# Kernel optimization log

Hardware: AMD Instinct MI355X
Metric: run time of the kernel (lower is better)

Reference implementation:

```python
import jax, jax.numpy as jnp
import numpy as np

EPS = 1e-6
NUM_GROUPS = 16


def group_norm(x, gamma, beta):
    # x: [B, C, H, W]
    B, C, H, W = x.shape
    xg = x.reshape(B, NUM_GROUPS, C // NUM_GROUPS, H, W)
    mean = xg.mean(axis=(2, 3, 4), keepdims=True)
    var = xg.var(axis=(2, 3, 4), keepdims=True)
    xg = (xg - mean) * jax.lax.rsqrt(var + EPS)
    x = xg.reshape(B, C, H, W)
    return x * gamma[None, :, None, None] + beta[None, :, None, None]


def conv1x1(x, w, b):
    # x: [B, C, H, W], w: [O, C], b: [O]
    return jnp.einsum('bchw,oc->bohw', x, w) + b[None, :, None, None]


def setup_inputs() -> dict:
    key = jax.random.key(0)
    ks = jax.random.split(key, 6)
    B, C, H, W = 8, 256, 64, 64
    s = 1.0 / np.sqrt(C)
    return {
        'x': jax.random.normal(ks[0], (B, C, H, W), dtype=jnp.float32),
        'gamma': jnp.ones((C,), jnp.float32),
        'beta': jnp.zeros((C,), jnp.float32),
        'wq': jax.random.normal(ks[1], (C, C), dtype=jnp.float32) * s,
        'bq': jnp.zeros((C,), jnp.float32),
        'wk': jax.random.normal(ks[2], (C, C), dtype=jnp.float32) * s,
        'bk': jnp.zeros((C,), jnp.float32),
        'wv': jax.random.normal(ks[3], (C, C), dtype=jnp.float32) * s,
        'bv': jnp.zeros((C,), jnp.float32),
        'wp': jax.random.normal(ks[4], (C, C), dtype=jnp.float32) * s,
        'bp': jnp.zeros((C,), jnp.float32),
    }


def reference(x, gamma, beta, wq, bq, wk, bk, wv, bv, wp, bp):
    B, C, H, W = x.shape
    identity = x
    h = group_norm(x, gamma, beta)
    q = conv1x1(h, wq, bq).reshape(B, C, H * W)  # [B, C, N]
    k = conv1x1(h, wk, bk).reshape(B, C, H * W)
    v = conv1x1(h, wv, bv).reshape(B, C, H * W)
    # alpha[b, i, j] = sum_c q[b, c, i] * k[b, c, j], scaled by C^-0.5
    alpha = jnp.einsum('bci,bcj->bij', q, k) * (C ** -0.5)
    alpha = jax.nn.softmax(alpha, axis=-1)
    # out[b, c, i] = sum_j v[b, c, j] * alpha[b, i, j]
    out = jnp.einsum('bcj,bij->bci', v, alpha).reshape(B, C, H, W)
    out = conv1x1(out, wp, bp)
    return identity + out
```

## Files before the change

kernel.cpp:

```cpp
#include <hip/hip_runtime.h>
#include <hip/hip_bf16.h>


typedef unsigned int u32;
typedef unsigned short u16;
typedef __bf16 bf16x8 __attribute__((ext_vector_type(8)));
typedef float f32x4 __attribute__((ext_vector_type(4)));
typedef float f32x16 __attribute__((ext_vector_type(16)));

#define GAS __attribute__((address_space(1)))
#define LAS __attribute__((address_space(3)))

__device__ __forceinline__ u16 f2bf(float f) {
  union { float f; u32 u; } v; v.f = f;
  return (u16)((v.u + 0x7fffu + ((v.u >> 16) & 1u)) >> 16);
}

__device__ __forceinline__ f32x16 mfma32(bf16x8 a, bf16x8 b, f32x16 c) {
  return __builtin_amdgcn_mfma_f32_32x32x16_bf16(a, b, c, 0, 0, 0);
}

template<int ITERS, int NT>
__device__ __forceinline__ void stage_lin(u16* lds, const u16* g, int tid) {
#pragma unroll
  for (int it = 0; it < ITERS; ++it) {
    int idx = it * NT + tid;
    const u16* src = g + (long)idx * 8;
    u16* dst = lds + (long)(idx & ~63) * 8;
    __builtin_amdgcn_global_load_lds((const GAS u32*)src, (LAS u32*)dst, 16, 0, 0);
  }
}

template<int ROWS, int NT>
__device__ __forceinline__ void stage_gran(u16* lds, const u16* g, int k0, int tid) {
  constexpr int ITERS = 4 * ROWS / NT;
#pragma unroll
  for (int it = 0; it < ITERS; ++it) {
    int gi = it * NT + tid;
    int row = gi & (ROWS - 1);
    int kh = gi / ROWS;
    const u16* src = g + (long)row * 256 + k0 + kh * 8;
    u16* dst = lds + (long)(gi & ~63) * 8;
    __builtin_amdgcn_global_load_lds((const GAS u32*)src, (LAS u32*)dst, 16, 0, 0);
  }
}

__global__ __launch_bounds__(256) void convert_w(
    const float* __restrict__ w0, const float* __restrict__ w1,
    const float* __restrict__ w2, const float* __restrict__ w3,
    u16* __restrict__ out) {
  int i = blockIdx.x * 256 + threadIdx.x;
  int seg = i >> 16, idx = i & 65535;
  const float* w = seg == 0 ? w0 : seg == 1 ? w1 : seg == 2 ? w2 : w3;
  out[i] = f2bf(w[idx]);
}

__global__ __launch_bounds__(256) void gn_kernel(
    const float* __restrict__ x, const float* __restrict__ gamma,
    const float* __restrict__ beta, u16* __restrict__ ht) {
  int tid = threadIdx.x;
  int b = blockIdx.x >> 4;
  int grp = blockIdx.x & 15;
  const float* xg = x + ((long)b * 256 + grp * 16) * 4096;

  float s = 0.f, ss = 0.f;
  const float4* x4 = (const float4*)xg;
#pragma unroll 4
  for (int it = 0; it < 64; ++it) {
    float4 v = x4[it * 256 + tid];
    s += v.x + v.y + v.z + v.w;
    ss += v.x * v.x + v.y * v.y + v.z * v.z + v.w * v.w;
  }
#pragma unroll
  for (int d = 1; d < 64; d <<= 1) {
    s += __shfl_xor(s, d);
    ss += __shfl_xor(ss, d);
  }
  __shared__ float red[10];
  int lane = tid & 63, wave = tid >> 6;
  if (lane == 0) { red[wave] = s; red[4 + wave] = ss; }
  __syncthreads();
  if (tid == 0) {
    float S = red[0] + red[1] + red[2] + red[3];
    float SS = red[4] + red[5] + red[6] + red[7];
    float mean = S * (1.f / 65536.f);
    float var = SS * (1.f / 65536.f) - mean * mean;
    red[8] = mean;
    red[9] = rsqrtf(var + 1e-6f);
  }
  __syncthreads();
  float mean = red[8], rstd = red[9];

  float a[16], bb[16];
#pragma unroll
  for (int c = 0; c < 16; ++c) {
    float gm = gamma[grp * 16 + c];
    float bt = beta[grp * 16 + c];
    a[c] = gm * rstd;
    bb[c] = bt - mean * a[c];
  }
  u16* hb = ht + (long)b * 4096 * 256 + grp * 16;
  for (int it = 0; it < 16; ++it) {
    int n = it * 256 + tid;
    __align__(16) u16 tmp[16];
#pragma unroll
    for (int c = 0; c < 16; ++c)
      tmp[c] = f2bf(xg[(long)c * 4096 + n] * a[c] + bb[c]);
    u16* dst = hb + (long)n * 256;
    ((uint4*)dst)[0] = ((uint4*)tmp)[0];
    ((uint4*)dst)[1] = ((uint4*)tmp)[1];
  }
}

__global__ __launch_bounds__(256, 2) void gemm_qkv(
    const u16* __restrict__ ht, const u16* __restrict__ wbf,
    u16* __restrict__ qtb, u16* __restrict__ ktb, u16* __restrict__ vcb,
    const float* __restrict__ bq, const float* __restrict__ bk,
    const float* __restrict__ bv) {
  __shared__ __align__(16) u16 as2[4 * 128 * 8];
  __shared__ __align__(16) u16 bs2[3][4 * 128 * 8];

  int tid = threadIdx.x;
  int lane = tid & 63;
  int h = lane >> 5, lr = lane & 31;
  int wave = tid >> 6;
  int wp = wave >> 1, wo = wave & 1;
  long mrow = (long)blockIdx.x * 128;
  int ob = blockIdx.y * 128;

  f32x16 zero16 = {0,0,0,0,0,0,0,0,0,0,0,0,0,0,0,0};
  f32x16 acc[3][2][2];
#pragma unroll
  for (int m = 0; m < 3; ++m)
#pragma unroll
    for (int p = 0; p < 2; ++p)
#pragma unroll
      for (int q = 0; q < 2; ++q) acc[m][p][q] = zero16;

  const u16* Ab = ht + mrow * 256;

  for (int step = 0; step < 8; ++step) {
    int k0 = step * 32;
    __syncthreads();
    stage_gran<128, 256>(as2, Ab, k0, tid);
    stage_gran<128, 256>(bs2[0], wbf + (long)ob * 256, k0, tid);
    stage_gran<128, 256>(bs2[1], wbf + 65536 + (long)ob * 256, k0, tid);
    stage_gran<128, 256>(bs2[2], wbf + 131072 + (long)ob * 256, k0, tid);
    __syncthreads();

#pragma unroll
    for (int ks = 0; ks < 2; ++ks) {
      int kg = (2 * ks + h) * 128;
      bf16x8 a0 = *(const bf16x8*)(as2 + (long)(kg + wp * 64 + lr) * 8);
      bf16x8 a1 = *(const bf16x8*)(as2 + (long)(kg + wp * 64 + 32 + lr) * 8);
      __builtin_amdgcn_s_setprio(1);
#pragma unroll
      for (int m = 0; m < 3; ++m) {
        bf16x8 b0 = *(const bf16x8*)(bs2[m] + (long)(kg + wo * 64 + lr) * 8);
        bf16x8 b1 = *(const bf16x8*)(bs2[m] + (long)(kg + wo * 64 + 32 + lr) * 8);
        acc[m][0][0] = mfma32(a0, b0, acc[m][0][0]);
        acc[m][0][1] = mfma32(a0, b1, acc[m][0][1]);
        acc[m][1][0] = mfma32(a1, b0, acc[m][1][0]);
        acc[m][1][1] = mfma32(a1, b1, acc[m][1][1]);
      }
      __builtin_amdgcn_s_setprio(0);
    }
  }

  const float QSC = 0.0625f * 1.44269504f;
  long b_ = mrow >> 12;
  int posb = (int)(mrow & 4095);
#pragma unroll
  for (int p = 0; p < 2; ++p)
#pragma unroll
    for (int q = 0; q < 2; ++q) {
      int o = ob + wo * 64 + q * 32 + lr;
      float bqv = bq[o], bkv = bk[o], bvv = bv[o];
      int posl0 = posb + wp * 64 + p * 32;
      int jt = posl0 >> 5;
      long tbase = b_ * 1048576 + (long)jt * 8192;
      long kbase = tbase + (o >> 3) * 256 + (o & 7);
      long vbase = tbase + (long)o * 8;
      long qrow0 = (mrow + wp * 64 + p * 32) * 256 + o;
#pragma unroll
      for (int quad = 0; quad < 4; ++quad) {
        __align__(8) u16 v4[4];
#pragma unroll
        for (int e = 0; e < 4; ++e) {
          int rloc = 8 * quad + 4 * h + e;
          float vq = acc[0][p][q][4 * quad + e];
          float vk = acc[1][p][q][4 * quad + e];
          float vv = acc[2][p][q][4 * quad + e];
          qtb[qrow0 + (long)rloc * 256] = f2bf((vq + bqv) * QSC);
          ktb[kbase + rloc * 8] = f2bf(vk + bkv);
          v4[e] = f2bf(vv + bvv);
        }
        int r0 = 8 * quad + 4 * h;
        *(uint2*)(vcb + vbase + ((r0 >> 3) & 3) * 2048 + (r0 & 7)) = *(uint2*)v4;
      }
    }
}

__global__ __launch_bounds__(256) void gemm_proj(
    const u16* __restrict__ Wp, const u16* __restrict__ ao,
    float* __restrict__ outp, const float* __restrict__ bias,
    const float* __restrict__ resid) {
  __shared__ __align__(16) u16 ws2[4 * 256 * 8];
  __shared__ __align__(16) u16 aos[4 * 64 * 8];

  int tid = threadIdx.x;
  int lane = tid & 63;
  int h = lane >> 5, lr = lane & 31;
  int wo = tid >> 6;
  long b = blockIdx.x & 7;
  int pos0 = (blockIdx.x >> 3) * 64;
  const u16* aob = ao + (b * 4096 + pos0) * 256;

  f32x16 zero16 = {0,0,0,0,0,0,0,0,0,0,0,0,0,0,0,0};
  f32x16 acc[2][2];
#pragma unroll
  for (int p = 0; p < 2; ++p)
#pragma unroll
    for (int q = 0; q < 2; ++q) acc[p][q] = zero16;

  for (int step = 0; step < 8; ++step) {
    int k0 = step * 32;
    __syncthreads();
    stage_gran<256, 256>(ws2, Wp, k0, tid);
    stage_gran<64, 256>(aos, aob, k0, tid);
    __syncthreads();

#pragma unroll
    for (int ks = 0; ks < 2; ++ks) {
      int kgw = (2 * ks + h) * 256;
      int kga = (2 * ks + h) * 64;
      bf16x8 w0 = *(const bf16x8*)(ws2 + (long)(kgw + wo * 64 + lr) * 8);
      bf16x8 w1 = *(const bf16x8*)(ws2 + (long)(kgw + wo * 64 + 32 + lr) * 8);
      bf16x8 o0 = *(const bf16x8*)(aos + (long)(kga + lr) * 8);
      bf16x8 o1 = *(const bf16x8*)(aos + (long)(kga + 32 + lr) * 8);
      __builtin_amdgcn_s_setprio(1);
      acc[0][0] = mfma32(w0, o0, acc[0][0]);
      acc[0][1] = mfma32(w0, o1, acc[0][1]);
      acc[1][0] = mfma32(w1, o0, acc[1][0]);
      acc[1][1] = mfma32(w1, o1, acc[1][1]);
      __builtin_amdgcn_s_setprio(0);
    }
  }

#pragma unroll
  for (int p = 0; p < 2; ++p)
#pragma unroll
    for (int q = 0; q < 2; ++q) {
      int pos = pos0 + q * 32 + lr;
#pragma unroll
      for (int quad = 0; quad < 4; ++quad)
#pragma unroll
        for (int e = 0; e < 4; ++e) {
          int o = wo * 64 + p * 32 + 8 * quad + 4 * h + e;
          long addr = b * 1048576 + (long)o * 4096 + pos;
          outp[addr] = acc[p][q][4 * quad + e] + bias[o] + resid[addr];
        }
    }
}

__global__ __launch_bounds__(256, 2) void attn_flash(
    const u16* __restrict__ qt, const u16* __restrict__ kgp,
    const u16* __restrict__ vgp, u16* __restrict__ part0, u16* __restrict__ part1,
    float2* __restrict__ ml0, float2* __restrict__ ml1) {
  __shared__ __align__(16) u16 ksT[2 * 8192];
  __shared__ __align__(16) u16 vsT[2 * 8192];
  __shared__ float fws[128];

  int tid = threadIdx.x;
  int lane = tid & 63;
  int h = lane >> 5, lr = lane & 31;
  int rg = tid >> 6;
  int bid = blockIdx.x;
  long b = bid & 7;
  int jhalf = (bid >> 3) & 1;
  int i0 = (bid >> 4) * 128;

  const u16* kb = kgp + b * 1048576 + (long)(jhalf * 64) * 8192;
  const u16* vb = vgp + b * 1048576 + (long)(jhalf * 64) * 8192;
  float* fw = fws + rg * 32;

  const u16* qrow = qt + ((b * 4096 + i0 + rg * 32 + lr) << 8) + h * 8;
  bf16x8 qreg[16];
#pragma unroll
  for (int kk = 0; kk < 16; ++kk)
    qreg[kk] = *(const bf16x8*)(qrow + kk * 16);

  f32x16 zero16 = {0,0,0,0,0,0,0,0,0,0,0,0,0,0,0,0};
  f32x16 acc[8];
#pragma unroll
  for (int ct = 0; ct < 8; ++ct) acc[ct] = zero16;
  float mrun = -3e38f, lsum = 0.f;

  stage_lin<4, 256>(ksT, kb, tid);
  stage_lin<4, 256>(vsT, vb, tid);

  for (int t = 0; t < 64; ++t) {
    int cur = t & 1, nxt = cur ^ 1;
    __builtin_amdgcn_s_barrier();
    __builtin_amdgcn_sched_barrier(0);
    if (t < 63) {
      stage_lin<4, 256>(ksT + nxt * 8192, kb + (long)(t + 1) * 8192, tid);
      stage_lin<4, 256>(vsT + nxt * 8192, vb + (long)(t + 1) * 8192, tid);
    }
    __builtin_amdgcn_sched_barrier(0);
    asm volatile("s_waitcnt vmcnt(8)" ::: "memory");
    __builtin_amdgcn_sched_barrier(0);
    __builtin_amdgcn_s_barrier();
    __builtin_amdgcn_sched_barrier(0);

    const u16* ksl = ksT + cur * 8192;
    const u16* vsl = vsT + cur * 8192;

    f32x16 sacc = zero16;
    __builtin_amdgcn_s_setprio(1);
#pragma unroll
    for (int kk = 0; kk < 16; ++kk) {
      bf16x8 kf = *(const bf16x8*)(ksl + ((2 * kk + h) * 32 + lr) * 8);
      sacc = mfma32(kf, qreg[kk], sacc);
    }
    __builtin_amdgcn_s_setprio(0);

    float m0 = fmaxf(fmaxf(sacc[0], sacc[1]), fmaxf(sacc[2], sacc[3]));
    float m1 = fmaxf(fmaxf(sacc[4], sacc[5]), fmaxf(sacc[6], sacc[7]));
    float m2 = fmaxf(fmaxf(sacc[8], sacc[9]), fmaxf(sacc[10], sacc[11]));
    float m3 = fmaxf(fmaxf(sacc[12], sacc[13]), fmaxf(sacc[14], sacc[15]));
    float mloc = fmaxf(fmaxf(m0, m1), fmaxf(m2, m3));
    mloc = fmaxf(mloc, __shfl_xor(mloc, 32));

    if (!__all(mloc - mrun <= 8.f)) {
      float mnew = fmaxf(mrun, mloc);
      float al = exp2f(mrun - mnew);
      mrun = mnew;
      lsum *= al;
      if (h == 0) fw[lr] = al;
      asm volatile("s_waitcnt lgkmcnt(0)" ::: "memory");
      f32x4 fq0 = *(const f32x4*)&fw[4 * h];
      f32x4 fq1 = *(const f32x4*)&fw[8 + 4 * h];
      f32x4 fq2 = *(const f32x4*)&fw[16 + 4 * h];
      f32x4 fq3 = *(const f32x4*)&fw[24 + 4 * h];
      f32x16 alv;
#pragma unroll
      for (int e = 0; e < 4; ++e) {
        alv[e] = fq0[e]; alv[4 + e] = fq1[e]; alv[8 + e] = fq2[e]; alv[12 + e] = fq3[e];
      }
#pragma unroll
      for (int ct = 0; ct < 8; ++ct) acc[ct] *= alv;
    }

    u32 u[8];
#pragma unroll
    for (int m = 0; m < 8; ++m) {
      float p0 = exp2f(sacc[2 * m] - mrun);
      float p1 = exp2f(sacc[2 * m + 1] - mrun);
      lsum += p0 + p1;
      asm volatile("v_cvt_pk_bf16_f32 %0, %1, %2" : "=v"(u[m]) : "v"(p0), "v"(p1));
    }
    u32 rv[4];
#pragma unroll
    for (int kt2 = 0; kt2 < 2; ++kt2)
#pragma unroll
      for (int idx = 0; idx < 2; ++idx) {
        u32 send = h ? u[4 * kt2 + idx] : u[4 * kt2 + 2 + idx];
        rv[kt2 * 2 + idx] = (u32)__shfl_xor((int)send, 32);
      }
    union { u32 wd[4]; bf16x8 v; } pf[2];
#pragma unroll
    for (int kt2 = 0; kt2 < 2; ++kt2) {
      pf[kt2].wd[0] = h ? rv[kt2 * 2] : u[4 * kt2];
      pf[kt2].wd[1] = h ? rv[kt2 * 2 + 1] : u[4 * kt2 + 1];
      pf[kt2].wd[2] = h ? u[4 * kt2 + 2] : rv[kt2 * 2];
      pf[kt2].wd[3] = h ? u[4 * kt2 + 3] : rv[kt2 * 2 + 1];
    }

    __builtin_amdgcn_s_setprio(1);
#pragma unroll
    for (int ct = 0; ct < 8; ++ct) {
      int c = ct * 32 + lr;
      bf16x8 vf0 = *(const bf16x8*)(vsl + ((long)h * 256 + c) * 8);
      bf16x8 vf1 = *(const bf16x8*)(vsl + ((long)(2 + h) * 256 + c) * 8);
      acc[ct] = mfma32(pf[0].v, vf0, acc[ct]);
      acc[ct] = mfma32(pf[1].v, vf1, acc[ct]);
    }
    __builtin_amdgcn_s_setprio(0);
    __builtin_amdgcn_sched_barrier(0);
  }

  lsum += __shfl_xor(lsum, 32);
  u16* pout = jhalf ? part1 : part0;
  float2* mlo = jhalf ? ml1 : ml0;
  if (h == 0)
    mlo[b * 4096 + i0 + rg * 32 + lr] = make_float2(mrun, lsum);
  u16* ob = pout + ((b * 4096 + i0 + rg * 32) << 8);
#pragma unroll
  for (int ct = 0; ct < 8; ++ct) {
    int c = ct * 32 + lr;
#pragma unroll
    for (int q = 0; q < 4; ++q)
#pragma unroll
      for (int e = 0; e < 4; ++e) {
        int i = 8 * q + 4 * h + e;
        ob[(long)i * 256 + c] = f2bf(acc[ct][4 * q + e]);
      }
  }
}

__global__ __launch_bounds__(256) void attn_merge(
    const u16* __restrict__ p0, const u16* __restrict__ p1,
    const float2* __restrict__ ml0, const float2* __restrict__ ml1,
    u16* __restrict__ out) {
  int tid = threadIdx.x;
  int row = blockIdx.x * 16 + (tid >> 4);
  int cs = (tid & 15) * 16;
  float2 a = ml0[row], c = ml1[row];
  float M = fmaxf(a.x, c.x);
  float w0 = exp2f(a.x - M), w1 = exp2f(c.x - M);
  float rl = 1.0f / (w0 * a.y + w1 * c.y);
  float f0 = w0 * rl, f1 = w1 * rl;

  long base = (long)row * 256 + cs;
  bf16x8 a0 = *(const bf16x8*)(p0 + base);
  bf16x8 a1 = *(const bf16x8*)(p0 + base + 8);
  bf16x8 c0 = *(const bf16x8*)(p1 + base);
  bf16x8 c1 = *(const bf16x8*)(p1 + base + 8);
  __align__(16) u16 o[16];
#pragma unroll
  for (int k = 0; k < 8; ++k) {
    o[k]     = f2bf(f0 * (float)a0[k] + f1 * (float)c0[k]);
    o[k + 8] = f2bf(f0 * (float)a1[k] + f1 * (float)c1[k]);
  }
  *(uint4*)(out + base) = ((uint4*)o)[0];
  *(uint4*)(out + base + 8) = ((uint4*)o)[1];
}

extern "C" void kernel_launch(void* const* d_in, const int* in_sizes, int n_in,
                              void* d_out, int out_size, void* d_ws, size_t ws_size,
                              hipStream_t stream) {
  const float* x     = (const float*)d_in[0];
  const float* gamma = (const float*)d_in[1];
  const float* beta  = (const float*)d_in[2];
  const float* wq = (const float*)d_in[3];
  const float* bq = (const float*)d_in[4];
  const float* wk = (const float*)d_in[5];
  const float* bk = (const float*)d_in[6];
  const float* wv = (const float*)d_in[7];
  const float* bv = (const float*)d_in[8];
  const float* wp = (const float*)d_in[9];
  const float* bp = (const float*)d_in[10];

  char* ws = (char*)d_ws;
  const long SZ = 16777216;
  u16* ht  = (u16*)(ws);
  u16* qtb = (u16*)(ws + SZ);
  u16* ktb = (u16*)(ws + 2 * SZ);
  u16* vcb = (u16*)(ws + 3 * SZ);
  u16* wbf = (u16*)(ws + 4 * SZ);
  u16* part0 = ht;
  u16* part1 = (u16*)d_out;
  float2* ml0 = (float2*)((char*)d_out + SZ);
  float2* ml1 = (float2*)((char*)d_out + SZ + 262144);

  convert_w<<<1024, 256, 0, stream>>>(wq, wk, wv, wp, wbf);
  gn_kernel<<<128, 256, 0, stream>>>(x, gamma, beta, ht);

  dim3 gq(256, 2, 1);
  gemm_qkv<<<gq, 256, 0, stream>>>(ht, wbf, qtb, ktb, vcb, bq, bk, bv);

  attn_flash<<<512, 256, 0, stream>>>(qtb, ktb, vcb, part0, part1, ml0, ml1);

  attn_merge<<<2048, 256, 0, stream>>>(part0, part1, ml0, ml1, qtb);

  dim3 gp(512, 1, 1);
  gemm_proj<<<gp, 256, 0, stream>>>(wbf + 3 * 65536, qtb, (float*)d_out, bp, x);
}
```

Before: 312.2 us.

## Double-buffer QKV GEMM staging and read V directly from global in attention

Result: slower. 398.0 us (+27.5%).

```diff
diff --git a/kernel.cpp b/kernel.cpp
--- a/kernel.cpp
+++ b/kernel.cpp
@@ -117,8 +117,8 @@
     u16* __restrict__ qtb, u16* __restrict__ ktb, u16* __restrict__ vcb,
     const float* __restrict__ bq, const float* __restrict__ bk,
     const float* __restrict__ bv) {
-  __shared__ __align__(16) u16 as2[4 * 128 * 8];
-  __shared__ __align__(16) u16 bs2[3][4 * 128 * 8];
+  __shared__ __align__(16) u16 as2[2][4 * 128 * 8];
+  __shared__ __align__(16) u16 bs2[2][3][4 * 128 * 8];
 
   int tid = threadIdx.x;
   int lane = tid & 63;
@@ -138,26 +138,40 @@
       for (int q = 0; q < 2; ++q) acc[m][p][q] = zero16;
 
   const u16* Ab = ht + mrow * 256;
+  const u16* W0 = wbf + (long)ob * 256;
+  const u16* W1 = wbf + 65536 + (long)ob * 256;
+  const u16* W2 = wbf + 131072 + (long)ob * 256;
+
+  stage_gran<128, 256>(as2[0], Ab, 0, tid);
+  stage_gran<128, 256>(bs2[0][0], W0, 0, tid);
+  stage_gran<128, 256>(bs2[0][1], W1, 0, tid);
+  stage_gran<128, 256>(bs2[0][2], W2, 0, tid);
 
   for (int step = 0; step < 8; ++step) {
-    int k0 = step * 32;
-    __syncthreads();
-    stage_gran<128, 256>(as2, Ab, k0, tid);
-    stage_gran<128, 256>(bs2[0], wbf + (long)ob * 256, k0, tid);
-    stage_gran<128, 256>(bs2[1], wbf + 65536 + (long)ob * 256, k0, tid);
-    stage_gran<128, 256>(bs2[2], wbf + 131072 + (long)ob * 256, k0, tid);
-    __syncthreads();
+    int cur = step & 1, nxt = cur ^ 1;
+    __builtin_amdgcn_s_barrier();
+    __builtin_amdgcn_sched_barrier(0);
+    int k0n = ((step + 1) & 7) * 32;
+    stage_gran<128, 256>(as2[nxt], Ab, k0n, tid);
+    stage_gran<128, 256>(bs2[nxt][0], W0, k0n, tid);
+    stage_gran<128, 256>(bs2[nxt][1], W1, k0n, tid);
+    stage_gran<128, 256>(bs2[nxt][2], W2, k0n, tid);
+    __builtin_amdgcn_sched_barrier(0);
+    asm volatile("s_waitcnt vmcnt(8)" ::: "memory");
+    __builtin_amdgcn_sched_barrier(0);
+    __builtin_amdgcn_s_barrier();
+    __builtin_amdgcn_sched_barrier(0);
 
 #pragma unroll
     for (int ks = 0; ks < 2; ++ks) {
       int kg = (2 * ks + h) * 128;
-      bf16x8 a0 = *(const bf16x8*)(as2 + (long)(kg + wp * 64 + lr) * 8);
-      bf16x8 a1 = *(const bf16x8*)(as2 + (long)(kg + wp * 64 + 32 + lr) * 8);
+      bf16x8 a0 = *(const bf16x8*)(as2[cur] + (long)(kg + wp * 64 + lr) * 8);
+      bf16x8 a1 = *(const bf16x8*)(as2[cur] + (long)(kg + wp * 64 + 32 + lr) * 8);
       __builtin_amdgcn_s_setprio(1);
 #pragma unroll
       for (int m = 0; m < 3; ++m) {
-        bf16x8 b0 = *(const bf16x8*)(bs2[m] + (long)(kg + wo * 64 + lr) * 8);
-        bf16x8 b1 = *(const bf16x8*)(bs2[m] + (long)(kg + wo * 64 + 32 + lr) * 8);
+        bf16x8 b0 = *(const bf16x8*)(bs2[cur][m] + (long)(kg + wo * 64 + lr) * 8);
+        bf16x8 b1 = *(const bf16x8*)(bs2[cur][m] + (long)(kg + wo * 64 + 32 + lr) * 8);
         acc[m][0][0] = mfma32(a0, b0, acc[m][0][0]);
         acc[m][0][1] = mfma32(a0, b1, acc[m][0][1]);
         acc[m][1][0] = mfma32(a1, b0, acc[m][1][0]);
@@ -166,6 +180,7 @@
       __builtin_amdgcn_s_setprio(0);
     }
   }
+  asm volatile("s_waitcnt vmcnt(0)" ::: "memory");
 
   const float QSC = 0.0625f * 1.44269504f;
   long b_ = mrow >> 12;
@@ -268,7 +283,6 @@
     const u16* __restrict__ vgp, u16* __restrict__ part0, u16* __restrict__ part1,
     float2* __restrict__ ml0, float2* __restrict__ ml1) {
   __shared__ __align__(16) u16 ksT[2 * 8192];
-  __shared__ __align__(16) u16 vsT[2 * 8192];
   __shared__ float fws[128];
 
   int tid = threadIdx.x;
@@ -297,24 +311,20 @@
   float mrun = -3e38f, lsum = 0.f;
 
   stage_lin<4, 256>(ksT, kb, tid);
-  stage_lin<4, 256>(vsT, vb, tid);
 
   for (int t = 0; t < 64; ++t) {
     int cur = t & 1, nxt = cur ^ 1;
     __builtin_amdgcn_s_barrier();
     __builtin_amdgcn_sched_barrier(0);
-    if (t < 63) {
-      stage_lin<4, 256>(ksT + nxt * 8192, kb + (long)(t + 1) * 8192, tid);
-      stage_lin<4, 256>(vsT + nxt * 8192, vb + (long)(t + 1) * 8192, tid);
-    }
-    __builtin_amdgcn_sched_barrier(0);
-    asm volatile("s_waitcnt vmcnt(8)" ::: "memory");
+    stage_lin<4, 256>(ksT + nxt * 8192, kb + (long)((t + 1) & 63) * 8192, tid);
+    __builtin_amdgcn_sched_barrier(0);
+    asm volatile("s_waitcnt vmcnt(4)" ::: "memory");
     __builtin_amdgcn_sched_barrier(0);
     __builtin_amdgcn_s_barrier();
     __builtin_amdgcn_sched_barrier(0);
 
     const u16* ksl = ksT + cur * 8192;
-    const u16* vsl = vsT + cur * 8192;
+    const u16* vt = vb + (long)t * 8192;
 
     f32x16 sacc = zero16;
     __builtin_amdgcn_s_setprio(1);
@@ -381,14 +391,15 @@
 #pragma unroll
     for (int ct = 0; ct < 8; ++ct) {
       int c = ct * 32 + lr;
-      bf16x8 vf0 = *(const bf16x8*)(vsl + ((long)h * 256 + c) * 8);
-      bf16x8 vf1 = *(const bf16x8*)(vsl + ((long)(2 + h) * 256 + c) * 8);
+      bf16x8 vf0 = *(const bf16x8*)(vt + ((long)h * 256 + c) * 8);
+      bf16x8 vf1 = *(const bf16x8*)(vt + ((long)(2 + h) * 256 + c) * 8);
       acc[ct] = mfma32(pf[0].v, vf0, acc[ct]);
       acc[ct] = mfma32(pf[1].v, vf1, acc[ct]);
     }
     __builtin_amdgcn_s_setprio(0);
     __builtin_amdgcn_sched_barrier(0);
   }
+  asm volatile("s_waitcnt vmcnt(0)" ::: "memory");
 
   lsum += __shfl_xor(lsum, 32);
   u16* pout = jhalf ? part1 : part0;
```
